# Performance work log

Hardware: AMD Instinct MI355X
Metric: run time of the kernel (lower is better)

Reference implementation:

```python
import jax, jax.numpy as jnp
import numpy as np
from jax import lax

B, N, C = 4, 9216, 64
HH = WW = 96
SR = 2
NUM_HEADS = 1
EPS = 1e-5


def setup_inputs() -> dict:
    key = jax.random.key(0)
    ks = jax.random.split(key, 8)
    w = 0.05  # keep logits in a stable range
    return {
        "x": jax.random.normal(ks[0], (B, N, C), jnp.float32),
        "conv_w": jax.random.normal(ks[1], (C, C, SR, SR), jnp.float32) * w,
        "conv_b": jnp.zeros((C,), jnp.float32),
        "bn_gamma": jnp.ones((C,), jnp.float32),
        "bn_beta": jnp.zeros((C,), jnp.float32),
        "bn_mean": jnp.zeros((C,), jnp.float32),
        "bn_var": jnp.ones((C,), jnp.float32),
        "ln_gamma": jnp.ones((C,), jnp.float32),
        "ln_beta": jnp.zeros((C,), jnp.float32),
        "wq": jax.random.normal(ks[2], (C, C), jnp.float32) * w,
        "wkv": jax.random.normal(ks[3], (2 * C, C), jnp.float32) * w,
        "wproj": jax.random.normal(ks[4], (C, C), jnp.float32) * w,
        "bproj": jnp.zeros((C,), jnp.float32),
        "H": HH,
        "W": WW,
    }


def reference(x, conv_w, conv_b, bn_gamma, bn_beta, bn_mean, bn_var,
              ln_gamma, ln_beta, wq, wkv, wproj, bproj, H, W):
    b, n, c = x.shape
    hd = c // NUM_HEADS
    scale = c ** (-0.5)  # torch uses full dim for the scale

    # q projection: [B, heads, N, hd]
    q = (x @ wq.T).reshape(b, n, NUM_HEADS, hd).transpose(0, 2, 1, 3)

    # spatial reduce: conv(stride=SR, kernel=SR) + BN (inference stats)
    x_ = x.transpose(0, 2, 1).reshape(b, c, H, W)
    x_ = lax.conv_general_dilated(x_, conv_w, (SR, SR), 'VALID',
                                  dimension_numbers=('NCHW', 'OIHW', 'NCHW'))
    x_ = x_ + conv_b[None, :, None, None]
    x_ = (x_ - bn_mean[None, :, None, None]) * lax.rsqrt(bn_var + EPS)[None, :, None, None]
    x_ = x_ * bn_gamma[None, :, None, None] + bn_beta[None, :, None, None]
    x_ = x_.reshape(b, c, -1).transpose(0, 2, 1)  # [B, N', C]

    # LayerNorm over channel dim
    mu = jnp.mean(x_, axis=-1, keepdims=True)
    var = jnp.var(x_, axis=-1, keepdims=True)
    x_ = (x_ - mu) * lax.rsqrt(var + EPS) * ln_gamma + ln_beta

    # kv projection: [2, B, heads, N', hd]
    kv = (x_ @ wkv.T).reshape(b, -1, 2, NUM_HEADS, hd).transpose(2, 0, 3, 1, 4)
    k, v = kv[0], kv[1]

    attn = jnp.einsum('bhnd,bhmd->bhnm', q, k) * scale  # [B,h,N,N']
    attn = jax.nn.softmax(attn, axis=-1)
    out = jnp.einsum('bhnm,bhmd->bhnd', attn, v)
    out = out.transpose(0, 2, 1, 3).reshape(b, n, c)
    return out @ wproj.T + bproj
```

## Files before the change

kernel.cpp:

```cpp
#include <hip/hip_runtime.h>

#define NB   4
#define NQ   9216
#define NKV  2304
#define NSPL 4
#define KSPL 576
#define EPS  1e-5f

typedef __attribute__((ext_vector_type(8)))  short          short8;
typedef __attribute__((ext_vector_type(8)))  unsigned short ushort8;
typedef __attribute__((ext_vector_type(4)))  unsigned short ushort4v;
typedef __attribute__((ext_vector_type(4)))  unsigned int   uint4v;
typedef __attribute__((ext_vector_type(4)))  float          f32x4;
typedef __attribute__((ext_vector_type(16))) float          f32x16;

static __device__ __forceinline__ f32x4 mfma16(ushort8 a, ushort8 b, f32x4 c) {
    return __builtin_amdgcn_mfma_f32_16x16x32_bf16(
        __builtin_bit_cast(short8, a), __builtin_bit_cast(short8, b), c, 0, 0, 0);
}
static __device__ __forceinline__ f32x16 mfma32(ushort8 a, ushort8 b, f32x16 c) {
    return __builtin_amdgcn_mfma_f32_32x32x16_bf16(
        __builtin_bit_cast(short8, a), __builtin_bit_cast(short8, b), c, 0, 0, 0);
}

static __device__ __forceinline__ unsigned short f2bf(float f) {
    unsigned int u = __float_as_uint(f);
    u = (u + 0x7fffu + ((u >> 16) & 1u)) >> 16;
    return (unsigned short)u;
}
static __device__ __forceinline__ float bf2f(unsigned short u) {
    return __uint_as_float(((unsigned int)u) << 16);
}
static __device__ __forceinline__ ushort4v pack4(f32x4 v) {
    ushort4v r; r.x = f2bf(v.x); r.y = f2bf(v.y); r.z = f2bf(v.z); r.w = f2bf(v.w);
    return r;
}
static __device__ __forceinline__ unsigned int cvt_pk_bf16(float lo, float hi) {
    unsigned int r;
    asm("v_cvt_pk_bf16_f32 %0, %1, %2" : "=v"(r) : "v"(lo), "v"(hi));
    return r;
}

#define QSCALE 0.18033688011112042f

__global__ __launch_bounds__(256) void prep_wt_kernel(
    const float* __restrict__ conv_w, const float* __restrict__ wkv,
    float* __restrict__ Wt2, float* __restrict__ Wkt2, float* __restrict__ Wvt2)
{
    const int idx = blockIdx.x * 256 + threadIdx.x;
    if (idx < 16384) {
        const int c = idx >> 8, r = idx & 255, o = r >> 2, pix = r & 3;
        Wt2[idx] = conv_w[o * 256 + c * 4 + pix];
    } else {
        const int i = idx - 16384;
        const int c4 = i >> 8, r = i & 255, o = r >> 2, j = r & 3;
        if (c4 < 16) Wkt2[c4 * 256 + o * 4 + j] = wkv[o * 64 + c4 * 4 + j];
        else         Wvt2[(c4 - 16) * 256 + o * 4 + j] = wkv[(64 + o) * 64 + (c4 - 16) * 4 + j];
    }
}

__global__ __launch_bounds__(256) void prep_fused_kernel(
    const float* __restrict__ x, const float* __restrict__ Wt2,
    const float* __restrict__ conv_b, const float* __restrict__ bn_g,
    const float* __restrict__ bn_b, const float* __restrict__ bn_m,
    const float* __restrict__ bn_v, const float* __restrict__ ln_g,
    const float* __restrict__ ln_b, const float* __restrict__ Wkt2,
    const float* __restrict__ Wvt2, const float* __restrict__ wq,
    const float* __restrict__ wproj,
    unsigned short* __restrict__ Kb, unsigned short* __restrict__ VTb,
    unsigned short* __restrict__ qb, unsigned short* __restrict__ wpb)
{
    __shared__ __align__(16) unsigned char ldsraw[20608];
    const int tid = threadIdx.x;

    if (blockIdx.x >= 1152) {
        const float4* s = (const float4*)(wproj + tid * 16);
        const float4 f0 = s[0], f1 = s[1], f2 = s[2], f3 = s[3];
        ushort8 a, b;
        a[0]=f2bf(f0.x); a[1]=f2bf(f0.y); a[2]=f2bf(f0.z); a[3]=f2bf(f0.w);
        a[4]=f2bf(f1.x); a[5]=f2bf(f1.y); a[6]=f2bf(f1.z); a[7]=f2bf(f1.w);
        b[0]=f2bf(f2.x); b[1]=f2bf(f2.y); b[2]=f2bf(f2.z); b[3]=f2bf(f2.w);
        b[4]=f2bf(f3.x); b[5]=f2bf(f3.y); b[6]=f2bf(f3.z); b[7]=f2bf(f3.w);
        *(ushort8*)(wpb + tid * 16)     = a;
        *(ushort8*)(wpb + tid * 16 + 8) = b;
        return;
    }

    if (blockIdx.x >= 576) {
        unsigned short* xbT = (unsigned short*)ldsraw;
        unsigned short* wqb = xbT + 4608;
        const long tok0 = (long)(blockIdx.x - 576) * 64;
        {
            const int tok = tid >> 2, c0 = (tid & 3) * 16;
            const float4* s = (const float4*)(x + (tok0 + tok) * 64 + c0);
            const float4 f0 = s[0], f1 = s[1], f2 = s[2], f3 = s[3];
            ushort8 a, b;
            a[0]=f2bf(f0.x); a[1]=f2bf(f0.y); a[2]=f2bf(f0.z); a[3]=f2bf(f0.w);
            a[4]=f2bf(f1.x); a[5]=f2bf(f1.y); a[6]=f2bf(f1.z); a[7]=f2bf(f1.w);
            b[0]=f2bf(f2.x); b[1]=f2bf(f2.y); b[2]=f2bf(f2.z); b[3]=f2bf(f2.w);
            b[4]=f2bf(f3.x); b[5]=f2bf(f3.y); b[6]=f2bf(f3.z); b[7]=f2bf(f3.w);
            *(ushort8*)(xbT + tok * 72 + c0)     = a;
            *(ushort8*)(xbT + tok * 72 + c0 + 8) = b;
            const float4* ws = (const float4*)(wq + tid * 16);
            const float4 g0 = ws[0], g1 = ws[1], g2 = ws[2], g3 = ws[3];
            ushort8 c, d;
            c[0]=f2bf(g0.x*QSCALE); c[1]=f2bf(g0.y*QSCALE); c[2]=f2bf(g0.z*QSCALE); c[3]=f2bf(g0.w*QSCALE);
            c[4]=f2bf(g1.x*QSCALE); c[5]=f2bf(g1.y*QSCALE); c[6]=f2bf(g1.z*QSCALE); c[7]=f2bf(g1.w*QSCALE);
            d[0]=f2bf(g2.x*QSCALE); d[1]=f2bf(g2.y*QSCALE); d[2]=f2bf(g2.z*QSCALE); d[3]=f2bf(g2.w*QSCALE);
            d[4]=f2bf(g3.x*QSCALE); d[5]=f2bf(g3.y*QSCALE); d[6]=f2bf(g3.z*QSCALE); d[7]=f2bf(g3.w*QSCALE);
            *(ushort8*)(wqb + tok * 72 + c0)     = c;
            *(ushort8*)(wqb + tok * 72 + c0 + 8) = d;
        }
        __syncthreads();
        const int w = tid >> 6, i = tid & 15, g = (tid >> 4) & 3;
        const ushort8 xb0 = *(const ushort8*)(xbT + (w * 16 + i) * 72 + g * 8);
        const ushort8 xb1 = *(const ushort8*)(xbT + (w * 16 + i) * 72 + 32 + g * 8);
        const f32x4 zero = {0.f, 0.f, 0.f, 0.f};
#pragma unroll
        for (int ot = 0; ot < 4; ++ot) {
            const ushort8 a0 = *(const ushort8*)(wqb + (ot * 16 + i) * 72 + g * 8);
            const ushort8 a1 = *(const ushort8*)(wqb + (ot * 16 + i) * 72 + 32 + g * 8);
            f32x4 acc = mfma16(a0, xb0, zero);
            acc = mfma16(a1, xb1, acc);
            *(ushort4v*)(qb + (tok0 + w * 16 + i) * 64 + ot * 16 + g * 4) = pack4(acc);
        }
        return;
    }

    float*  xs    = (float*)ldsraw;
    float*  ys    = (float*)(ldsraw + 16384);
    float2* stats = (float2*)(ldsraw + 20480);
    const int b  = blockIdx.x / 144;
    const int p0 = (blockIdx.x % 144) * 16;
    {
        const int r = tid >> 2, kk = tid & 3;
        const int tok = r >> 2, pix = r & 3;
        const int p = p0 + tok;
        const int i = p / 48, j = p - i * 48;
        const int n = (2 * i + (pix >> 1)) * 96 + 2 * j + (pix & 1);
        const float* src = x + ((long)b * NQ + n) * 64 + kk * 16;
#pragma unroll
        for (int cc = 0; cc < 4; ++cc) {
            const float4 v = *(const float4*)(src + cc * 4);
            const int c = kk * 16 + cc * 4;
            xs[(c + 0) * 64 + r] = v.x;
            xs[(c + 1) * 64 + r] = v.y;
            xs[(c + 2) * 64 + r] = v.z;
            xs[(c + 3) * 64 + r] = v.w;
        }
    }
    __syncthreads();
    const int o = tid & 63, tg = tid >> 6;
    {
        float a0 = 0.f, a1 = 0.f, a2 = 0.f, a3 = 0.f;
        const float* xbase = xs + tg * 16;
#pragma unroll 8
        for (int c = 0; c < 64; ++c) {
            const float4 w4 = *(const float4*)(Wt2 + c * 256 + o * 4);
            const float* xr = xbase + c * 64;
            const float4 x0 = *(const float4*)(xr + 0);
            const float4 x1 = *(const float4*)(xr + 4);
            const float4 x2 = *(const float4*)(xr + 8);
            const float4 x3 = *(const float4*)(xr + 12);
            a0 += w4.x * x0.x + w4.y * x0.y + w4.z * x0.z + w4.w * x0.w;
            a1 += w4.x * x1.x + w4.y * x1.y + w4.z * x1.z + w4.w * x1.w;
            a2 += w4.x * x2.x + w4.y * x2.y + w4.z * x2.z + w4.w * x2.w;
            a3 += w4.x * x3.x + w4.y * x3.y + w4.z * x3.z + w4.w * x3.w;
        }
        const float rs = rsqrtf(bn_v[o] + EPS);
        const float sh = conv_b[o] - bn_m[o];
        const float gg = bn_g[o], bb = bn_b[o];
        ys[(tg * 4 + 0) * 64 + o] = (a0 + sh) * rs * gg + bb;
        ys[(tg * 4 + 1) * 64 + o] = (a1 + sh) * rs * gg + bb;
        ys[(tg * 4 + 2) * 64 + o] = (a2 + sh) * rs * gg + bb;
        ys[(tg * 4 + 3) * 64 + o] = (a3 + sh) * rs * gg + bb;
    }
    __syncthreads();
    {
        const int tk = tid >> 4, s = tid & 15;
        const float4 yv = *(const float4*)(ys + tk * 64 + s * 4);
        float s1 = yv.x + yv.y + yv.z + yv.w;
        float s2 = yv.x * yv.x + yv.y * yv.y + yv.z * yv.z + yv.w * yv.w;
#pragma unroll
        for (int mm = 1; mm <= 8; mm <<= 1) {
            s1 += __shfl_xor(s1, mm);
            s2 += __shfl_xor(s2, mm);
        }
        if (s == 0) {
            const float mu = s1 * (1.f / 64.f);
            const float var = s2 * (1.f / 64.f) - mu * mu;
            stats[tk] = make_float2(mu, rsqrtf(var + EPS));
        }
    }
    __syncthreads();
    {
        const float lg = ln_g[o], lb = ln_b[o];
#pragma unroll
        for (int qq = 0; qq < 4; ++qq) {
            const int tt = tg * 4 + qq;
            const float2 st = stats[tt];
            ys[tt * 64 + o] = (ys[tt * 64 + o] - st.x) * st.y * lg + lb;
        }
    }
    __syncthreads();
    {
        float k0 = 0.f, k1 = 0.f, k2 = 0.f, k3 = 0.f;
        float v0 = 0.f, v1 = 0.f, v2 = 0.f, v3 = 0.f;
        const float* zbase = ys + tg * 256;
#pragma unroll
        for (int c4 = 0; c4 < 16; ++c4) {
            const float4 wk = *(const float4*)(Wkt2 + c4 * 256 + o * 4);
            const float4 wv = *(const float4*)(Wvt2 + c4 * 256 + o * 4);
            const float4 z0 = *(const float4*)(zbase + 0 * 64 + c4 * 4);
            const float4 z1 = *(const float4*)(zbase + 1 * 64 + c4 * 4);
            const float4 z2 = *(const float4*)(zbase + 2 * 64 + c4 * 4);
            const float4 z3 = *(const float4*)(zbase + 3 * 64 + c4 * 4);
            k0 += wk.x * z0.x + wk.y * z0.y + wk.z * z0.z + wk.w * z0.w;
            k1 += wk.x * z1.x + wk.y * z1.y + wk.z * z1.z + wk.w * z1.w;
            k2 += wk.x * z2.x + wk.y * z2.y + wk.z * z2.z + wk.w * z2.w;
            k3 += wk.x * z3.x + wk.y * z3.y + wk.z * z3.z + wk.w * z3.w;
            v0 += wv.x * z0.x + wv.y * z0.y + wv.z * z0.z + wv.w * z0.w;
            v1 += wv.x * z1.x + wv.y * z1.y + wv.z * z1.z + wv.w * z1.w;
            v2 += wv.x * z2.x + wv.y * z2.y + wv.z * z2.z + wv.w * z2.w;
            v3 += wv.x * z3.x + wv.y * z3.y + wv.z * z3.z + wv.w * z3.w;
        }
        const long pg = (long)b * NKV + p0 + tg * 4;
        Kb[(pg + 0) * 64 + o] = f2bf(k0);
        Kb[(pg + 1) * 64 + o] = f2bf(k1);
        Kb[(pg + 2) * 64 + o] = f2bf(k2);
        Kb[(pg + 3) * 64 + o] = f2bf(k3);
        unsigned short* vt = VTb + ((long)b * 64 + o) * NKV + p0 + tg * 4;
        vt[0] = f2bf(v0); vt[1] = f2bf(v1); vt[2] = f2bf(v2); vt[3] = f2bf(v3);
    }
}

__global__ __launch_bounds__(256, 5) void attn_kernel(
    const unsigned short* __restrict__ qb, const unsigned short* __restrict__ Kb,
    const unsigned short* __restrict__ VTb, unsigned short* __restrict__ Opart,
    float* __restrict__ Ml)
{
    __shared__ __align__(16) unsigned short smem[9728];
    unsigned short* ldsK  = smem;
    unsigned short* ldsVT = smem + 4608;

    const int tid  = threadIdx.x;
    const int lane = tid & 63;
    const int q5 = lane & 31;
    const int hi = lane >> 5;
    const int wid = tid >> 6;
    const int s   = blockIdx.x / 288;
    const int rem = blockIdx.x % 288;
    const int b   = rem / 72;
    const int q0  = (rem % 72) * 128 + wid * 32;
    const int kbase = s * KSPL;

    const unsigned short* qrow = qb + ((long)b * NQ + q0 + q5) * 64 + hi * 8;
    const ushort8 qf0 = *(const ushort8*)(qrow);
    const ushort8 qf1 = *(const ushort8*)(qrow + 16);
    const ushort8 qf2 = *(const ushort8*)(qrow + 32);
    const ushort8 qf3 = *(const ushort8*)(qrow + 48);

    const int kr   = tid >> 3;
    const int slot = (kr & ~12) | ((kr & 8) >> 1) | ((kr & 4) << 1);
    const unsigned short* gK  = Kb  + ((long)b * NKV + kbase + kr) * 64 + (tid & 7) * 8;
    const unsigned short* gVT = VTb + ((long)b * 64 + (tid >> 2)) * NKV + kbase + (tid & 3) * 8;
    const int lkw = slot * 72 + (tid & 7) * 8;
    const int lvw = (tid >> 2) * 40 + (tid & 3) * 8;

    float lsum = 0.f;
    f32x16 oc0, oc1;
#pragma unroll
    for (int i = 0; i < 16; ++i) { oc0[i] = 0.f; oc1[i] = 0.f; }

    ushort8 rk = *(const ushort8*)gK;
    ushort8 rv = *(const ushort8*)gVT;
    *(ushort8*)(ldsK + lkw)  = rk;
    *(ushort8*)(ldsVT + lvw) = rv;
    __syncthreads();

    for (int t = 0; t < 18; ++t) {
        const unsigned short* K_ = ldsK  + (t & 1) * 2304;
        const unsigned short* V_ = ldsVT + (t & 1) * 2560;
        if (t < 17) {
            rk = *(const ushort8*)(gK + (long)(t + 1) * 2048);
            rv = *(const ushort8*)(gVT + (t + 1) * 32);
        }
        f32x16 sS;
#pragma unroll
        for (int i = 0; i < 16; ++i) sS[i] = 0.f;
        {
            const int ar = q5 * 72 + hi * 8;
            sS = mfma32(*(const ushort8*)(K_ + ar),      qf0, sS);
            sS = mfma32(*(const ushort8*)(K_ + ar + 16), qf1, sS);
            sS = mfma32(*(const ushort8*)(K_ + ar + 32), qf2, sS);
            sS = mfma32(*(const ushort8*)(K_ + ar + 48), qf3, sS);
        }
        unsigned int pa[8];
        float l0 = 0.f;
#pragma unroll
        for (int i = 0; i < 8; ++i) {
            const float ea = __builtin_amdgcn_exp2f(sS[2 * i]);
            const float eb = __builtin_amdgcn_exp2f(sS[2 * i + 1]);
            l0 += ea + eb;
            pa[i] = cvt_pk_bf16(ea, eb);
        }
        lsum += l0;
        const uint4v w0 = {pa[0], pa[1], pa[2], pa[3]};
        const uint4v w1 = {pa[4], pa[5], pa[6], pa[7]};
        const ushort8 pf0 = __builtin_bit_cast(ushort8, w0);
        const ushort8 pf1 = __builtin_bit_cast(ushort8, w1);
        {
            const int vr = q5 * 40 + hi * 8;
            oc0 = mfma32(*(const ushort8*)(V_ + vr),             pf0, oc0);
            oc0 = mfma32(*(const ushort8*)(V_ + vr + 16),        pf1, oc0);
            oc1 = mfma32(*(const ushort8*)(V_ + 1280 + vr),      pf0, oc1);
            oc1 = mfma32(*(const ushort8*)(V_ + 1280 + vr + 16), pf1, oc1);
        }
        if (t < 17) {
            *(ushort8*)(ldsK + ((t + 1) & 1) * 2304 + lkw)  = rk;
            *(ushort8*)(ldsVT + ((t + 1) & 1) * 2560 + lvw) = rv;
        }
        __syncthreads();
    }

    const float tot = lsum + __shfl_xor(lsum, 32);
    const float inv = 1.f / tot;
    unsigned short* ob = Opart + (((long)s * NB + b) * NQ + q0 + q5) * 64 + 4 * hi;
#pragma unroll
    for (int j = 0; j < 4; ++j) {
        const f32x4 v0 = {oc0[4 * j] * inv, oc0[4 * j + 1] * inv,
                          oc0[4 * j + 2] * inv, oc0[4 * j + 3] * inv};
        const f32x4 v1 = {oc1[4 * j] * inv, oc1[4 * j + 1] * inv,
                          oc1[4 * j + 2] * inv, oc1[4 * j + 3] * inv};
        *(ushort4v*)(ob + 8 * j)      = pack4(v0);
        *(ushort4v*)(ob + 32 + 8 * j) = pack4(v1);
    }
    if (hi == 0) Ml[((long)s * NB + b) * NQ + q0 + q5] = tot;
}

__global__ __launch_bounds__(256) void combine_kernel(
    const unsigned short* __restrict__ Opart, const float* __restrict__ Ml,
    const unsigned short* __restrict__ wpb, const float* __restrict__ bproj,
    float* __restrict__ out)
{
    __shared__ unsigned short pe[4][16 * 72];
    const int tid = threadIdx.x;
    const int w = tid >> 6, lq = tid & 15, g = (tid >> 4) & 3;
    const int b  = blockIdx.x / 144;
    const int q0 = (blockIdx.x % 144) * 64;
    const long q = (long)q0 + w * 16 + lq;

    float wt[NSPL], wsum = 0.f;
#pragma unroll
    for (int sp = 0; sp < NSPL; ++sp) {
        wt[sp] = Ml[((long)sp * NB + b) * NQ + q];
        wsum += wt[sp];
    }
    float acc[16];
#pragma unroll
    for (int j = 0; j < 16; ++j) acc[j] = 0.f;
#pragma unroll
    for (int sp = 0; sp < NSPL; ++sp) {
        const unsigned short* op = Opart + (((long)sp * NB + b) * NQ + q) * 64 + g * 16;
        const ushort8 u0 = *(const ushort8*)op;
        const ushort8 u1 = *(const ushort8*)(op + 8);
        const float wg = wt[sp];
#pragma unroll
        for (int j = 0; j < 8; ++j) acc[j]     += wg * bf2f(u0[j]);
#pragma unroll
        for (int j = 0; j < 8; ++j) acc[8 + j] += wg * bf2f(u1[j]);
    }
    const float sc = 1.f / wsum;
    ushort8 e0, e1;
#pragma unroll
    for (int j = 0; j < 8; ++j) { e0[j] = f2bf(acc[j] * sc); e1[j] = f2bf(acc[8 + j] * sc); }
    unsigned short* pew = pe[w];
    *(ushort8*)(pew + lq * 72 + g * 16)     = e0;
    *(ushort8*)(pew + lq * 72 + g * 16 + 8) = e1;
    const ushort8 af0 = *(const ushort8*)(pew + lq * 72 + g * 8);
    const ushort8 af1 = *(const ushort8*)(pew + lq * 72 + 32 + g * 8);
    const f32x4 zero = {0.f, 0.f, 0.f, 0.f};
#pragma unroll
    for (int et = 0; et < 4; ++et) {
        const unsigned short* wr = wpb + (et * 16 + lq) * 64 + g * 8;
        const ushort8 w0 = *(const ushort8*)wr;
        const ushort8 w1 = *(const ushort8*)(wr + 32);
        f32x4 acc2 = mfma16(af0, w0, zero);
        acc2 = mfma16(af1, w1, acc2);
        const float bias = bproj[et * 16 + lq];
        float* orow = out + ((long)b * NQ + q0 + w * 16 + 4 * g) * 64 + et * 16 + lq;
        orow[0]   = acc2.x + bias;
        orow[64]  = acc2.y + bias;
        orow[128] = acc2.z + bias;
        orow[192] = acc2.w + bias;
    }
}

extern "C" void kernel_launch(void* const* d_in, const int* in_sizes, int n_in,
                              void* d_out, int out_size, void* d_ws, size_t ws_size,
                              hipStream_t stream)
{
    (void)in_sizes; (void)n_in; (void)out_size; (void)ws_size;
    const float* x      = (const float*)d_in[0];
    const float* conv_w = (const float*)d_in[1];
    const float* conv_b = (const float*)d_in[2];
    const float* bn_g   = (const float*)d_in[3];
    const float* bn_b   = (const float*)d_in[4];
    const float* bn_m   = (const float*)d_in[5];
    const float* bn_v   = (const float*)d_in[6];
    const float* ln_g   = (const float*)d_in[7];
    const float* ln_b   = (const float*)d_in[8];
    const float* wq     = (const float*)d_in[9];
    const float* wkv    = (const float*)d_in[10];
    const float* wproj  = (const float*)d_in[11];
    const float* bpr    = (const float*)d_in[12];

    unsigned short* qb    = (unsigned short*)d_ws;
    unsigned short* Kb    = qb + 2359296;
    unsigned short* VTb   = Kb + 589824;
    unsigned short* wpb   = VTb + 589824;
    unsigned short* Opart = wpb + 4096;
    float*          Ml    = (float*)(Opart + 9437184);
    float*          Wt2   = Ml + 147456;
    float*          Wkt2  = Wt2 + 16384;
    float*          Wvt2  = Wkt2 + 4096;

    prep_wt_kernel<<<96, 256, 0, stream>>>(conv_w, wkv, Wt2, Wkt2, Wvt2);
    prep_fused_kernel<<<1153, 256, 0, stream>>>(x, Wt2, conv_b, bn_g, bn_b, bn_m,
                                                bn_v, ln_g, ln_b, Wkt2, Wvt2, wq, wproj,
                                                Kb, VTb, qb, wpb);
    attn_kernel<<<1152, 256, 0, stream>>>(qb, Kb, VTb, Opart, Ml);
    combine_kernel<<<576, 256, 0, stream>>>(Opart, Ml, wpb, bpr, (float*)d_out);
}
```

Baseline: 149.6 us.

## Use bf16 MFMA for spatial-reduce conv with BN folded into weights

The stride-2 conv in the prep kernel moves from scalar fp32 FMAs to bf16 16x16x32 MFMAs. BatchNorm scale is folded into bf16 conv weights and the bias precomputed in the weight-prep kernel. The x tile is staged in LDS row-major with padding (stride 68), and the combine kernel's output projection swaps MFMA operands so each lane writes a float4 instead of strided scalars. This reduces conv compute and makes output stores coalesced, at the cost of bf16 rounding in the conv input and weights.

```diff
diff --git a/kernel.cpp b/kernel.cpp
--- a/kernel.cpp
+++ b/kernel.cpp
@@ -45,32 +45,39 @@
 
 __global__ __launch_bounds__(256) void prep_wt_kernel(
     const float* __restrict__ conv_w, const float* __restrict__ wkv,
-    float* __restrict__ Wt2, float* __restrict__ Wkt2, float* __restrict__ Wvt2)
+    const float* __restrict__ conv_b, const float* __restrict__ bn_g,
+    const float* __restrict__ bn_b, const float* __restrict__ bn_m,
+    const float* __restrict__ bn_v,
+    unsigned short* __restrict__ Wbp, float* __restrict__ bnb,
+    float* __restrict__ Wkt2, float* __restrict__ Wvt2)
 {
     const int idx = blockIdx.x * 256 + threadIdx.x;
     if (idx < 16384) {
-        const int c = idx >> 8, r = idx & 255, o = r >> 2, pix = r & 3;
-        Wt2[idx] = conv_w[o * 256 + c * 4 + pix];
-    } else {
-        const int i = idx - 16384;
-        const int c4 = i >> 8, r = i & 255, o = r >> 2, j = r & 3;
+        const int p = idx >> 12, r = idx & 4095, o = r >> 6, c = r & 63;
+        const float rs = rsqrtf(bn_v[o] + EPS) * bn_g[o];
+        Wbp[idx] = f2bf(conv_w[o * 256 + c * 4 + p] * rs);
+    } else if (idx < 16448) {
+        const int o = idx - 16384;
+        const float rs = rsqrtf(bn_v[o] + EPS) * bn_g[o];
+        bnb[o] = (conv_b[o] - bn_m[o]) * rs + bn_b[o];
+    } else if (idx < 24640) {
+        const int i2 = idx - 16448;
+        const int c4 = i2 >> 8, r = i2 & 255, o = r >> 2, j = r & 3;
         if (c4 < 16) Wkt2[c4 * 256 + o * 4 + j] = wkv[o * 64 + c4 * 4 + j];
         else         Wvt2[(c4 - 16) * 256 + o * 4 + j] = wkv[(64 + o) * 64 + (c4 - 16) * 4 + j];
     }
 }
 
 __global__ __launch_bounds__(256) void prep_fused_kernel(
-    const float* __restrict__ x, const float* __restrict__ Wt2,
-    const float* __restrict__ conv_b, const float* __restrict__ bn_g,
-    const float* __restrict__ bn_b, const float* __restrict__ bn_m,
-    const float* __restrict__ bn_v, const float* __restrict__ ln_g,
+    const float* __restrict__ x, const unsigned short* __restrict__ Wbp,
+    const float* __restrict__ bnb, const float* __restrict__ ln_g,
     const float* __restrict__ ln_b, const float* __restrict__ Wkt2,
     const float* __restrict__ Wvt2, const float* __restrict__ wq,
     const float* __restrict__ wproj,
     unsigned short* __restrict__ Kb, unsigned short* __restrict__ VTb,
     unsigned short* __restrict__ qb, unsigned short* __restrict__ wpb)
 {
-    __shared__ __align__(16) unsigned char ldsraw[20608];
+    __shared__ __align__(16) unsigned char ldsraw[21888];
     const int tid = threadIdx.x;
 
     if (blockIdx.x >= 1152) {
@@ -128,57 +135,54 @@
     }
 
     float*  xs    = (float*)ldsraw;
-    float*  ys    = (float*)(ldsraw + 16384);
-    float2* stats = (float2*)(ldsraw + 20480);
+    float*  ys    = (float*)(ldsraw + 17408);
+    float2* stats = (float2*)(ldsraw + 21760);
     const int b  = blockIdx.x / 144;
     const int p0 = (blockIdx.x % 144) * 16;
     {
-        const int r = tid >> 2, kk = tid & 3;
+        const int r = tid >> 2, cq = (tid & 3) * 16;
         const int tok = r >> 2, pix = r & 3;
         const int p = p0 + tok;
-        const int i = p / 48, j = p - i * 48;
-        const int n = (2 * i + (pix >> 1)) * 96 + 2 * j + (pix & 1);
-        const float* src = x + ((long)b * NQ + n) * 64 + kk * 16;
-#pragma unroll
-        for (int cc = 0; cc < 4; ++cc) {
-            const float4 v = *(const float4*)(src + cc * 4);
-            const int c = kk * 16 + cc * 4;
-            xs[(c + 0) * 64 + r] = v.x;
-            xs[(c + 1) * 64 + r] = v.y;
-            xs[(c + 2) * 64 + r] = v.z;
-            xs[(c + 3) * 64 + r] = v.w;
-        }
+        const int ii = p / 48, jj = p - ii * 48;
+        const int n = (2 * ii + (pix >> 1)) * 96 + 2 * jj + (pix & 1);
+        const float4* src = (const float4*)(x + ((long)b * NQ + n) * 64 + cq);
+        float* dst = xs + r * 68 + cq;
+        *(float4*)(dst)      = src[0];
+        *(float4*)(dst + 4)  = src[1];
+        *(float4*)(dst + 8)  = src[2];
+        *(float4*)(dst + 12) = src[3];
     }
     __syncthreads();
+    const int lane = tid & 63, wid = tid >> 6;
     const int o = tid & 63, tg = tid >> 6;
     {
-        float a0 = 0.f, a1 = 0.f, a2 = 0.f, a3 = 0.f;
-        const float* xbase = xs + tg * 16;
-#pragma unroll 8
-        for (int c = 0; c < 64; ++c) {
-            const float4 w4 = *(const float4*)(Wt2 + c * 256 + o * 4);
-            const float* xr = xbase + c * 64;
-            const float4 x0 = *(const float4*)(xr + 0);
-            const float4 x1 = *(const float4*)(xr + 4);
-            const float4 x2 = *(const float4*)(xr + 8);
-            const float4 x3 = *(const float4*)(xr + 12);
-            a0 += w4.x * x0.x + w4.y * x0.y + w4.z * x0.z + w4.w * x0.w;
-            a1 += w4.x * x1.x + w4.y * x1.y + w4.z * x1.z + w4.w * x1.w;
-            a2 += w4.x * x2.x + w4.y * x2.y + w4.z * x2.z + w4.w * x2.w;
-            a3 += w4.x * x3.x + w4.y * x3.y + w4.z * x3.z + w4.w * x3.w;
-        }
-        const float rs = rsqrtf(bn_v[o] + EPS);
-        const float sh = conv_b[o] - bn_m[o];
-        const float gg = bn_g[o], bb = bn_b[o];
-        ys[(tg * 4 + 0) * 64 + o] = (a0 + sh) * rs * gg + bb;
-        ys[(tg * 4 + 1) * 64 + o] = (a1 + sh) * rs * gg + bb;
-        ys[(tg * 4 + 2) * 64 + o] = (a2 + sh) * rs * gg + bb;
-        ys[(tg * 4 + 3) * 64 + o] = (a3 + sh) * rs * gg + bb;
+        const int i = lane & 15, g4 = lane >> 4;
+        f32x4 yacc = {0.f, 0.f, 0.f, 0.f};
+#pragma unroll
+        for (int p = 0; p < 4; ++p) {
+            const float* xr = xs + (i * 4 + p) * 68 + g4 * 8;
+            const float4 xa = *(const float4*)(xr);
+            const float4 xb = *(const float4*)(xr + 4);
+            const float4 xc = *(const float4*)(xr + 32);
+            const float4 xd = *(const float4*)(xr + 36);
+            uint4v u0 = {cvt_pk_bf16(xa.x, xa.y), cvt_pk_bf16(xa.z, xa.w),
+                         cvt_pk_bf16(xb.x, xb.y), cvt_pk_bf16(xb.z, xb.w)};
+            uint4v u1 = {cvt_pk_bf16(xc.x, xc.y), cvt_pk_bf16(xc.z, xc.w),
+                         cvt_pk_bf16(xd.x, xd.y), cvt_pk_bf16(xd.z, xd.w)};
+            const unsigned short* wb = Wbp + p * 4096 + (wid * 16 + i) * 64 + g4 * 8;
+            const ushort8 a0 = *(const ushort8*)(wb);
+            const ushort8 a1 = *(const ushort8*)(wb + 32);
+            yacc = mfma16(a0, __builtin_bit_cast(ushort8, u0), yacc);
+            yacc = mfma16(a1, __builtin_bit_cast(ushort8, u1), yacc);
+        }
+        const float4 b4 = *(const float4*)(bnb + wid * 16 + 4 * g4);
+        float4 st = make_float4(yacc.x + b4.x, yacc.y + b4.y, yacc.z + b4.z, yacc.w + b4.w);
+        *(float4*)(ys + i * 68 + wid * 16 + 4 * g4) = st;
     }
     __syncthreads();
     {
         const int tk = tid >> 4, s = tid & 15;
-        const float4 yv = *(const float4*)(ys + tk * 64 + s * 4);
+        const float4 yv = *(const float4*)(ys + tk * 68 + s * 4);
         float s1 = yv.x + yv.y + yv.z + yv.w;
         float s2 = yv.x * yv.x + yv.y * yv.y + yv.z * yv.z + yv.w * yv.w;
 #pragma unroll
@@ -199,22 +203,22 @@
         for (int qq = 0; qq < 4; ++qq) {
             const int tt = tg * 4 + qq;
             const float2 st = stats[tt];
-            ys[tt * 64 + o] = (ys[tt * 64 + o] - st.x) * st.y * lg + lb;
+            ys[tt * 68 + o] = (ys[tt * 68 + o] - st.x) * st.y * lg + lb;
         }
     }
     __syncthreads();
     {
         float k0 = 0.f, k1 = 0.f, k2 = 0.f, k3 = 0.f;
         float v0 = 0.f, v1 = 0.f, v2 = 0.f, v3 = 0.f;
-        const float* zbase = ys + tg * 256;
+        const float* zbase = ys + tg * 4 * 68;
 #pragma unroll
         for (int c4 = 0; c4 < 16; ++c4) {
             const float4 wk = *(const float4*)(Wkt2 + c4 * 256 + o * 4);
             const float4 wv = *(const float4*)(Wvt2 + c4 * 256 + o * 4);
-            const float4 z0 = *(const float4*)(zbase + 0 * 64 + c4 * 4);
-            const float4 z1 = *(const float4*)(zbase + 1 * 64 + c4 * 4);
-            const float4 z2 = *(const float4*)(zbase + 2 * 64 + c4 * 4);
-            const float4 z3 = *(const float4*)(zbase + 3 * 64 + c4 * 4);
+            const float4 z0 = *(const float4*)(zbase + 0 * 68 + c4 * 4);
+            const float4 z1 = *(const float4*)(zbase + 1 * 68 + c4 * 4);
+            const float4 z2 = *(const float4*)(zbase + 2 * 68 + c4 * 4);
+            const float4 z3 = *(const float4*)(zbase + 3 * 68 + c4 * 4);
             k0 += wk.x * z0.x + wk.y * z0.y + wk.z * z0.z + wk.w * z0.w;
             k1 += wk.x * z1.x + wk.y * z1.y + wk.z * z1.z + wk.w * z1.w;
             k2 += wk.x * z2.x + wk.y * z2.y + wk.z * z2.z + wk.w * z2.w;
@@ -385,14 +389,12 @@
         const unsigned short* wr = wpb + (et * 16 + lq) * 64 + g * 8;
         const ushort8 w0 = *(const ushort8*)wr;
         const ushort8 w1 = *(const ushort8*)(wr + 32);
-        f32x4 acc2 = mfma16(af0, w0, zero);
-        acc2 = mfma16(af1, w1, acc2);
-        const float bias = bproj[et * 16 + lq];
-        float* orow = out + ((long)b * NQ + q0 + w * 16 + 4 * g) * 64 + et * 16 + lq;
-        orow[0]   = acc2.x + bias;
-        orow[64]  = acc2.y + bias;
-        orow[128] = acc2.z + bias;
-        orow[192] = acc2.w + bias;
+        f32x4 acc2 = mfma16(w0, af0, zero);
+        acc2 = mfma16(w1, af1, acc2);
+        const float4 b4 = *(const float4*)(bproj + et * 16 + 4 * g);
+        float* orow = out + ((long)b * NQ + q0 + w * 16 + lq) * 64 + et * 16 + 4 * g;
+        *(float4*)orow = make_float4(acc2.x + b4.x, acc2.y + b4.y,
+                                     acc2.z + b4.z, acc2.w + b4.w);
     }
 }
 
@@ -421,14 +423,15 @@
     unsigned short* wpb   = VTb + 589824;
     unsigned short* Opart = wpb + 4096;
     float*          Ml    = (float*)(Opart + 9437184);
-    float*          Wt2   = Ml + 147456;
-    float*          Wkt2  = Wt2 + 16384;
+    float*          Wkt2  = Ml + 147456;
     float*          Wvt2  = Wkt2 + 4096;
-
-    prep_wt_kernel<<<96, 256, 0, stream>>>(conv_w, wkv, Wt2, Wkt2, Wvt2);
-    prep_fused_kernel<<<1153, 256, 0, stream>>>(x, Wt2, conv_b, bn_g, bn_b, bn_m,
-                                                bn_v, ln_g, ln_b, Wkt2, Wvt2, wq, wproj,
-                                                Kb, VTb, qb, wpb);
+    unsigned short* Wbp   = (unsigned short*)(Wvt2 + 4096);
+    float*          bnb   = (float*)(Wbp + 16384);
+
+    prep_wt_kernel<<<97, 256, 0, stream>>>(conv_w, wkv, conv_b, bn_g, bn_b, bn_m,
+                                           bn_v, Wbp, bnb, Wkt2, Wvt2);
+    prep_fused_kernel<<<1153, 256, 0, stream>>>(x, Wbp, bnb, ln_g, ln_b, Wkt2, Wvt2,
+                                                wq, wproj, Kb, VTb, qb, wpb);
     attn_kernel<<<1152, 256, 0, stream>>>(qb, Kb, VTb, Opart, Ml);
     combine_kernel<<<576, 256, 0, stream>>>(Opart, Ml, wpb, bpr, (float*)d_out);
 }
```

Result: faster. 140.2 us (-6.2%).
